# Kernel tuning notes

Measured on AMD Instinct MI355X. Metric: run time of the kernel, lower is better.

## Reference

```python
import jax, jax.numpy as jnp
import numpy as np

U = 100000          # unique pillars
N = 2 * U           # voxels (2 per pillar -> unq_cnt==2, mask all True)
NUM_BINS = 32       # z bins
C_IN = 5
C_HID = 32          # out_channels // 2 in conv1d MLP
C_OUT = 64
R = 4               # channel-attention reduction
K = 7               # bin-attention conv kernel


def setup_inputs() -> dict:
    key = jax.random.key(0)
    ks = jax.random.split(key, 12)
    voxel_features = jax.random.normal(ks[0], (N, C_IN), jnp.float32)
    # each pillar p owns voxels 2p, 2p+1 placed in two distinct bins -> no scatter collision
    bins = (jnp.arange(N, dtype=jnp.int32) % NUM_BINS)
    voxel_coords = jnp.zeros((N, 4), jnp.int32).at[:, 1].set(bins)
    unq_coords = jnp.arange(U, dtype=jnp.int32)
    unq_inv = jnp.arange(N, dtype=jnp.int32) // 2
    unq_cnt = jnp.full((U,), 2, jnp.int32)
    s = 0.3
    return {
        'voxel_features': voxel_features,
        'voxel_coords': voxel_coords,
        'unq_coords': unq_coords,
        'unq_inv': unq_inv,
        'unq_cnt': unq_cnt,
        # up_dimension MLP (Linear(5,32) -> relu -> Linear(32,64))
        'W1': jax.random.normal(ks[1], (C_IN, C_HID), jnp.float32) * s,
        'b1': jnp.zeros((C_HID,), jnp.float32),
        'W2': jax.random.normal(ks[2], (C_HID, C_OUT), jnp.float32) * s,
        'b2': jnp.zeros((C_OUT,), jnp.float32),
        # ZBAM channel-attention shared MLP
        'Wc1': jax.random.normal(ks[3], (C_OUT, C_OUT // R), jnp.float32) * s,
        'bc1': jnp.zeros((C_OUT // R,), jnp.float32),
        'Wc2': jax.random.normal(ks[4], (C_OUT // R, C_OUT), jnp.float32) * s,
        'bc2': jnp.zeros((C_OUT,), jnp.float32),
        # ZBAM bin (spatial) attention: conv1d over bins, 2->1 channels, kernel 7
        'Wsp': jax.random.normal(ks[5], (1, 2, K), jnp.float32) * s,
        'bsp': jnp.zeros((1,), jnp.float32),
    }


def _cbam_forward(voxel_features, W1, b1, W2, b2, Wc1, bc1, Wc2, bc2, Wsp, bsp,
                  voxel_coords, unq_coords, unq_inv, unq_cnt):
    n_pillars = unq_coords.shape[0]
    # --- binning: scatter voxels into (pillar, z-bin) slots ---
    src = jnp.zeros((n_pillars, NUM_BINS, voxel_features.shape[1]), voxel_features.dtype)
    src = src.at[unq_inv, voxel_coords[:, 1]].set(voxel_features)
    occupied_mask = unq_cnt >= 2  # all True by construction -> src[mask] == src
    # --- up_dimension MLP: (U, bins, 5) -> (U, bins, 64) ---
    x = jax.nn.relu(src @ W1 + b1) @ W2 + b2
    x = jnp.transpose(x, (0, 2, 1))  # (U, C, bins)
    # --- ZBAM channel attention ---
    avg_p = x.mean(axis=2)
    max_p = x.max(axis=2)
    mlp = lambda v: jax.nn.relu(v @ Wc1 + bc1) @ Wc2 + bc2
    att_c = jax.nn.sigmoid(mlp(avg_p) + mlp(max_p))  # (U, C)
    x = x * att_c[:, :, None]
    # --- ZBAM bin attention (conv over z-bins) ---
    s = jnp.stack([x.mean(axis=1), x.max(axis=1)], axis=1)  # (U, 2, bins)
    att_s = jax.lax.conv_general_dilated(
        s, Wsp, window_strides=(1,), padding=[(K // 2, K // 2)],
        dimension_numbers=('NCH', 'OIH', 'NCH')) + bsp  # (U, 1, bins)
    x = x * jax.nn.sigmoid(att_s)
    # --- max-pool over bins ---
    return x.max(axis=2), occupied_mask


def reference(voxel_features, voxel_coords, unq_coords, unq_inv, unq_cnt,
              W1, b1, W2, b2, Wc1, bc1, Wc2, bc2, Wsp, bsp):
    return _cbam_forward(voxel_features, W1, b1, W2, b2, Wc1, bc1, Wc2, bc2,
                         Wsp, bsp, voxel_coords, unq_coords, unq_inv, unq_cnt)
```

## Files before the change

kernel.cpp:

```cpp
#include <hip/hip_runtime.h>
#include <math.h>


#define CO 64

__device__ __forceinline__ float sgm(float x) {
  return 1.0f / (1.0f + __expf(-x));
}
template <int PAT>
__device__ __forceinline__ float qadd(float s) {
  int t = __builtin_amdgcn_update_dpp(0, __builtin_bit_cast(int, s),
                                      PAT, 0xf, 0xf, true);
  return s + __builtin_bit_cast(float, t);
}
template <int PAT>
__device__ __forceinline__ float qmaxd(float m) {
  int t = __builtin_amdgcn_update_dpp(__builtin_bit_cast(int, m),
                                      __builtin_bit_cast(int, m),
                                      PAT, 0xf, 0xf, false);
  return fmaxf(m, __builtin_bit_cast(float, t));
}
template <int PAT>
__device__ __forceinline__ float qmind(float m) {
  int t = __builtin_amdgcn_update_dpp(__builtin_bit_cast(int, m),
                                      __builtin_bit_cast(int, m),
                                      PAT, 0xf, 0xf, false);
  return fminf(m, __builtin_bit_cast(float, t));
}
__device__ __forceinline__ float qsum4(float s) { return qadd<0x4E>(qadd<0xB1>(s)); }
__device__ __forceinline__ float qmax4(float m) { return qmaxd<0x4E>(qmaxd<0xB1>(m)); }
__device__ __forceinline__ float qmin4(float m) { return qmind<0x4E>(qmind<0xB1>(m)); }
__device__ __forceinline__ void drain_lds() {
  __builtin_amdgcn_wave_barrier();
  __builtin_amdgcn_s_waitcnt(0xC07F);
  __builtin_amdgcn_wave_barrier();
}

__global__ __launch_bounds__(256) void pack_kernel(
    const float* __restrict__ vf, const int* __restrict__ vcoord,
    const int* __restrict__ unq_inv, float* __restrict__ pvox, int n) {
  int i = blockIdx.x * blockDim.x + threadIdx.x;
  if (i >= n) return;
  int p = unq_inv[i];
  int slot = (i > 0 && unq_inv[i - 1] == p) ? 1 : 0;
  float* dst = pvox + 8 * (size_t)(2 * p + slot);
#pragma unroll
  for (int k = 0; k < 5; ++k) dst[k] = vf[5 * i + k];
  ((int*)dst)[5] = vcoord[4 * i + 1];
}

__global__ __launch_bounds__(256) void cbam_kernel(
    const float* __restrict__ pvox, const int* __restrict__ unq_cnt,
    const float* __restrict__ W1, const float* __restrict__ b1,
    const float* __restrict__ W2, const float* __restrict__ b2,
    const float* __restrict__ Wc1, const float* __restrict__ bc1,
    const float* __restrict__ Wc2, const float* __restrict__ bc2,
    const float* __restrict__ Wsp, const float* __restrict__ bsp,
    float* __restrict__ out, int U) {
  __shared__ __align__(16) float w2b[2176];
  __shared__ __align__(16) float wc1b[1024];
  __shared__ __align__(16) float wc2b[1024];
  __shared__ __align__(16) float c0b[64], b2b[64], bc2b[64], bc1b[16];
  __shared__ __align__(16) float wsmx[64];
  __shared__ __align__(16) float wtab[16];
  __shared__ __align__(16) float hbuf[4][1152];

  const int tid = threadIdx.x;

  for (int i = tid; i < 2048; i += 256) w2b[(i >> 6) * 68 + (i & 63)] = W2[i];
  for (int i = tid; i < 1024; i += 256) wc1b[i] = Wc1[i];
  for (int i = tid; i < 1024; i += 256) wc2b[i] = Wc2[(i & 15) * 64 + (i >> 4)];
  if (tid < 64) { b2b[tid] = b2[tid]; bc2b[tid] = bc2[tid]; }
  if (tid < 16) bc1b[tid] = bc1[tid];
  if (tid < 32) {
    float sm = 0.0f, sx = 0.0f;
    for (int k = 0; k < 7; ++k)
      if ((unsigned)(tid + k - 3) < 32u) { sm += Wsp[k]; sx += Wsp[7 + k]; }
    wsmx[2 * tid] = sm; wsmx[2 * tid + 1] = sx;
  }
  if (tid < 8) {
    float a = 0.0f, b = 0.0f;
    if (tid < 7) { a = Wsp[tid]; b = Wsp[7 + tid]; }
    wtab[2 * tid] = a; wtab[2 * tid + 1] = b;
  }
  __syncthreads();
  if (tid < 64) {
    float c = b2b[tid];
    for (int j = 0; j < 32; ++j) c += fmaxf(b1[j], 0.0f) * w2b[j * 68 + tid];
    c0b[tid] = c;
  }
  __syncthreads();

  const int wv = tid >> 6, lane = tid & 63;
  const int P0 = (blockIdx.x * 4 + wv) * 16;
  if (P0 >= U) return;
  float* const hb = hbuf[wv];

  {
    const int j32 = lane & 31, vh = lane >> 5;
    float w1r[5];
#pragma unroll
    for (int i = 0; i < 5; ++i) w1r[i] = W1[i * 32 + j32];
    const float b1r = b1[j32];
    const float4* pv4 = (const float4*)pvox;
    const int vmax = 2 * U - 1;
#pragma unroll
    for (int v = 0; v < 16; ++v) {
      int vg = 2 * P0 + 16 * vh + v;
      vg = vg < vmax ? vg : vmax;
      float4 g1 = pv4[2 * vg];
      float4 g2 = pv4[2 * vg + 1];
      float h = b1r + g1.x * w1r[0] + g1.y * w1r[1] + g1.z * w1r[2] +
                g1.w * w1r[3] + g2.x * w1r[4];
      hb[(16 * vh + v) * 36 + j32] = fmaxf(h, 0.0f);
    }
  }
  drain_lds();

  const int q = lane & 3, pp = lane >> 2;
  const int pg = P0 + pp;
  const int pc = pg < U ? pg : (U - 1);
  const int cnt = unq_cnt[pc];
  const bool has2 = (cnt >= 2);
  const int* pvi = (const int*)pvox;
  const int b0 = pvi[(size_t)(2 * pc) * 8 + 5] & 31;
  const int b1raw = pvi[(size_t)(2 * pc + 1) * 8 + 5];
  const int b1e = has2 ? (b1raw & 31) : 64;

  float y0[16], y1[16];
  const float4* b2b4 = (const float4*)b2b;
#pragma unroll
  for (int kb = 0; kb < 4; ++kb) {
    float4 w = b2b4[q * 4 + kb];
    y0[4 * kb] = w.x; y0[4 * kb + 1] = w.y; y0[4 * kb + 2] = w.z; y0[4 * kb + 3] = w.w;
    y1[4 * kb] = w.x; y1[4 * kb + 1] = w.y; y1[4 * kb + 2] = w.z; y1[4 * kb + 3] = w.w;
  }
  const float4* hb4 = (const float4*)hb;
  const float4* w2b4 = (const float4*)w2b;
#pragma unroll
  for (int jb = 0; jb < 8; ++jb) {
    float4 h0 = hb4[(2 * pp) * 9 + jb];
    float4 h1 = hb4[(2 * pp + 1) * 9 + jb];
    float h0a[4] = {h0.x, h0.y, h0.z, h0.w};
    float h1a[4] = {h1.x, h1.y, h1.z, h1.w};
#pragma unroll
    for (int jj = 0; jj < 4; ++jj) {
      const int j = 4 * jb + jj;
#pragma unroll
      for (int kb = 0; kb < 4; ++kb) {
        float4 w = w2b4[17 * j + 4 * q + kb];
        y0[4 * kb]     += h0a[jj] * w.x; y0[4 * kb + 1] += h0a[jj] * w.y;
        y0[4 * kb + 2] += h0a[jj] * w.z; y0[4 * kb + 3] += h0a[jj] * w.w;
        y1[4 * kb]     += h1a[jj] * w.x; y1[4 * kb + 1] += h1a[jj] * w.y;
        y1[4 * kb + 2] += h1a[jj] * w.z; y1[4 * kb + 3] += h1a[jj] * w.w;
      }
    }
  }
#pragma unroll
  for (int k = 0; k < 16; ++k) y1[k] = has2 ? y1[k] : y0[k];

  float ha[16] = {0}, hm[16] = {0};
  const float kf = has2 ? 30.0f : 31.0f;
  const float inv32 = 1.0f / 32.0f;
  const float4* c04 = (const float4*)c0b;
  const float4* wc14 = (const float4*)wc1b;
#pragma unroll
  for (int kb = 0; kb < 4; ++kb) {
    float4 cq = c04[q * 4 + kb];
    float c0a[4] = {cq.x, cq.y, cq.z, cq.w};
#pragma unroll
    for (int i = 0; i < 4; ++i) {
      const int k = 4 * kb + i;
      const float c0v = c0a[i];
      const float sumy = y0[k] + (has2 ? y1[k] : 0.0f);
      const float avg = fmaf(c0v, kf, sumy) * inv32;
      const float mxv = fmaxf(fmaxf(y0[k], y1[k]), c0v);
#pragma unroll
      for (int jb = 0; jb < 4; ++jb) {
        float4 w = wc14[(16 * q + k) * 4 + jb];
        ha[4 * jb]     += avg * w.x; ha[4 * jb + 1] += avg * w.y;
        ha[4 * jb + 2] += avg * w.z; ha[4 * jb + 3] += avg * w.w;
        hm[4 * jb]     += mxv * w.x; hm[4 * jb + 1] += mxv * w.y;
        hm[4 * jb + 2] += mxv * w.z; hm[4 * jb + 3] += mxv * w.w;
      }
    }
  }
  float g[16];
  const float4* bc14 = (const float4*)bc1b;
#pragma unroll
  for (int jb = 0; jb < 4; ++jb) {
    float4 bb = bc14[jb];
    float bba[4] = {bb.x, bb.y, bb.z, bb.w};
#pragma unroll
    for (int i = 0; i < 4; ++i) {
      const int j = 4 * jb + i;
      const float sa = qsum4(ha[j]) + bba[i];
      const float sm = qsum4(hm[j]) + bba[i];
      g[j] = fmaxf(sa, 0.0f) + fmaxf(sm, 0.0f);
    }
  }

  float attc[16];
  float sc = 0.0f, mc = -3.0e38f;
  float sy0 = 0.0f, my0 = -3.0e38f, sy1 = 0.0f, my1 = -3.0e38f;
  const float4* wc24 = (const float4*)wc2b;
  const float4* bc24 = (const float4*)bc2b;
#pragma unroll
  for (int kb = 0; kb < 4; ++kb) {
    float4 cq = c04[q * 4 + kb];
    float4 bq = bc24[q * 4 + kb];
    float c0a[4] = {cq.x, cq.y, cq.z, cq.w};
    float b2a[4] = {bq.x, bq.y, bq.z, bq.w};
#pragma unroll
    for (int i = 0; i < 4; ++i) {
      const int k = 4 * kb + i;
      float pre = 2.0f * b2a[i];
#pragma unroll
      for (int jb = 0; jb < 4; ++jb) {
        float4 w = wc24[(16 * q + k) * 4 + jb];
        pre += g[4 * jb] * w.x + g[4 * jb + 1] * w.y +
               g[4 * jb + 2] * w.z + g[4 * jb + 3] * w.w;
      }
      const float a = sgm(pre);
      attc[k] = a;
      const float pc0 = a * c0a[i], py0 = a * y0[k], py1 = a * y1[k];
      sc += pc0;  mc = fmaxf(mc, pc0);
      sy0 += py0; my0 = fmaxf(my0, py0);
      sy1 += py1; my1 = fmaxf(my1, py1);
    }
  }
  sc = qsum4(sc);   mc = qmax4(mc);
  sy0 = qsum4(sy0); my0 = qmax4(my0);
  sy1 = qsum4(sy1); my1 = qmax4(my1);

  const float inv64 = 1.0f / 64.0f;
  const float Mn = sc * inv64, Mx = mc;
  const float dm0 = (sy0 - sc) * inv64, dx0 = my0 - mc;
  const float dm1 = (sy1 - sc) * inv64, dx1 = my1 - mc;
  const float bspr = bsp[0];
  const float2* ws2 = (const float2*)wsmx;
  const float2* wt2 = (const float2*)wtab;
  float maxE = -3.0e38f, minE = 3.0e38f, sv0 = -3.0e38f, sv1 = -3.0e38f;
#pragma unroll
  for (int k = 0; k < 8; ++k) {
    const int b = 8 * q + k;
    float2 ws = ws2[b];
    float acc = bspr + Mn * ws.x + Mx * ws.y;
    int k0 = b0 - b + 3;  k0 = ((unsigned)k0 <= 6u) ? k0 : 7;
    int k1 = b1e - b + 3; k1 = ((unsigned)k1 <= 6u) ? k1 : 7;
    float2 w0 = wt2[k0];
    float2 w1v = wt2[k1];
    acc += dm0 * w0.x + dx0 * w0.y + dm1 * w1v.x + dx1 * w1v.y;
    const bool o0 = (b == b0), o1 = (b == b1e);
    const bool oc = o0 || o1;
    maxE = fmaxf(maxE, oc ? -3.0e38f : acc);
    minE = fminf(minE, oc ?  3.0e38f : acc);
    sv0 = o0 ? acc : sv0;
    sv1 = o1 ? acc : sv1;
  }
  maxE = qmax4(maxE); minE = qmin4(minE);
  sv0 = qmax4(sv0);   sv1 = qmax4(sv1);
  const float sig0 = sgm(sv0);
  const float sig1 = has2 ? sgm(sv1) : sig0;
  const float sE = sgm(maxE), sI = sgm(minE);

  if (pg < U) {
    float4* ov = (float4*)(out + (size_t)pg * CO + 16 * q);
#pragma unroll
    for (int kb = 0; kb < 4; ++kb) {
      float4 cq = c04[q * 4 + kb];
      float c0a[4] = {cq.x, cq.y, cq.z, cq.w};
      float rr[4];
#pragma unroll
      for (int i = 0; i < 4; ++i) {
        const int k = 4 * kb + i;
        const float c0v = c0a[i];
        const float sel = (c0v >= 0.0f) ? sE : sI;
        const float m = fmaxf(fmaxf(y0[k] * sig0, y1[k] * sig1), c0v * sel);
        rr[i] = attc[k] * m;
      }
      float4 r; r.x = rr[0]; r.y = rr[1]; r.z = rr[2]; r.w = rr[3];
      ov[kb] = r;
    }
    if (q == 0) out[(size_t)U * CO + pg] = has2 ? 1.0f : 0.0f;
  }
}

extern "C" void kernel_launch(void* const* d_in, const int* in_sizes, int n_in,
                              void* d_out, int out_size, void* d_ws, size_t ws_size,
                              hipStream_t stream) {
  const float* vf      = (const float*)d_in[0];
  const int*   vcoord  = (const int*)d_in[1];
  const int*   unq_inv = (const int*)d_in[3];
  const int*   unq_cnt = (const int*)d_in[4];
  const float* W1  = (const float*)d_in[5];
  const float* b1  = (const float*)d_in[6];
  const float* W2  = (const float*)d_in[7];
  const float* b2  = (const float*)d_in[8];
  const float* Wc1 = (const float*)d_in[9];
  const float* bc1 = (const float*)d_in[10];
  const float* Wc2 = (const float*)d_in[11];
  const float* bc2 = (const float*)d_in[12];
  const float* Wsp = (const float*)d_in[13];
  const float* bsp = (const float*)d_in[14];

  const int N = in_sizes[3];
  const int U = in_sizes[4];

  float* pvox = (float*)d_ws;

  pack_kernel<<<(N + 255) / 256, 256, 0, stream>>>(vf, vcoord, unq_inv, pvox, N);

  const int waves = (U + 15) / 16;
  const int blocks = (waves + 3) / 4;
  cbam_kernel<<<blocks, 256, 0, stream>>>(
      pvox, unq_cnt, W1, b1, W2, b2, Wc1, bc1, Wc2, bc2, Wsp, bsp,
      (float*)d_out, U);
}
```

Before: 155.5 us.

## Make CBAM kernel persistent with grid-stride waves and reorder LDS layouts

The main kernel now launches a capped grid of 1024 blocks, and each wave loops over 16-pillar groups in grid-stride fashion. The per-block weight staging into shared memory and the W1 register loads now happen once per wave rather than once per group. The hidden-activation rows and the Wc1/Wc2 shared-memory layouts are permuted, intended to reduce LDS bank conflicts, and the hidden-row reads are software-prefetched one step ahead. The cost is fewer resident blocks, which may reduce latency hiding, plus an extra LDS drain per loop iteration.

After: 147.6 us. 5.1% less time.

```diff
diff --git a/kernel.cpp b/kernel.cpp
--- a/kernel.cpp
+++ b/kernel.cpp
@@ -56,7 +56,7 @@
     const float* __restrict__ Wc1, const float* __restrict__ bc1,
     const float* __restrict__ Wc2, const float* __restrict__ bc2,
     const float* __restrict__ Wsp, const float* __restrict__ bsp,
-    float* __restrict__ out, int U) {
+    float* __restrict__ out, int U, int ngroups, int totalWaves) {
   __shared__ __align__(16) float w2b[2176];
   __shared__ __align__(16) float wc1b[1024];
   __shared__ __align__(16) float wc2b[1024];
@@ -68,8 +68,11 @@
   const int tid = threadIdx.x;
 
   for (int i = tid; i < 2048; i += 256) w2b[(i >> 6) * 68 + (i & 63)] = W2[i];
-  for (int i = tid; i < 1024; i += 256) wc1b[i] = Wc1[i];
-  for (int i = tid; i < 1024; i += 256) wc2b[i] = Wc2[(i & 15) * 64 + (i >> 4)];
+  for (int i = tid; i < 1024; i += 256) {
+    int ch = i >> 4, j = i & 15, qq = ch >> 4, k = ch & 15;
+    wc1b[(4 * k + qq) * 16 + j] = Wc1[i];
+    wc2b[(4 * k + qq) * 16 + j] = Wc2[j * 64 + ch];
+  }
   if (tid < 64) { b2b[tid] = b2[tid]; bc2b[tid] = bc2[tid]; }
   if (tid < 16) bc1b[tid] = bc1[tid];
   if (tid < 32) {
@@ -92,197 +95,210 @@
   __syncthreads();
 
   const int wv = tid >> 6, lane = tid & 63;
-  const int P0 = (blockIdx.x * 4 + wv) * 16;
-  if (P0 >= U) return;
+  const int wave0 = blockIdx.x * 4 + wv;
   float* const hb = hbuf[wv];
 
-  {
-    const int j32 = lane & 31, vh = lane >> 5;
-    float w1r[5];
-#pragma unroll
-    for (int i = 0; i < 5; ++i) w1r[i] = W1[i * 32 + j32];
-    const float b1r = b1[j32];
-    const float4* pv4 = (const float4*)pvox;
-    const int vmax = 2 * U - 1;
-#pragma unroll
-    for (int v = 0; v < 16; ++v) {
-      int vg = 2 * P0 + 16 * vh + v;
-      vg = vg < vmax ? vg : vmax;
-      float4 g1 = pv4[2 * vg];
-      float4 g2 = pv4[2 * vg + 1];
-      float h = b1r + g1.x * w1r[0] + g1.y * w1r[1] + g1.z * w1r[2] +
-                g1.w * w1r[3] + g2.x * w1r[4];
-      hb[(16 * vh + v) * 36 + j32] = fmaxf(h, 0.0f);
-    }
-  }
-  drain_lds();
+  const int j32 = lane & 31, vh = lane >> 5;
+  float w1r[5];
+#pragma unroll
+  for (int i = 0; i < 5; ++i) w1r[i] = W1[i * 32 + j32];
+  const float b1r = b1[j32];
 
   const int q = lane & 3, pp = lane >> 2;
-  const int pg = P0 + pp;
-  const int pc = pg < U ? pg : (U - 1);
-  const int cnt = unq_cnt[pc];
-  const bool has2 = (cnt >= 2);
-  const int* pvi = (const int*)pvox;
-  const int b0 = pvi[(size_t)(2 * pc) * 8 + 5] & 31;
-  const int b1raw = pvi[(size_t)(2 * pc + 1) * 8 + 5];
-  const int b1e = has2 ? (b1raw & 31) : 64;
-
-  float y0[16], y1[16];
-  const float4* b2b4 = (const float4*)b2b;
-#pragma unroll
-  for (int kb = 0; kb < 4; ++kb) {
-    float4 w = b2b4[q * 4 + kb];
-    y0[4 * kb] = w.x; y0[4 * kb + 1] = w.y; y0[4 * kb + 2] = w.z; y0[4 * kb + 3] = w.w;
-    y1[4 * kb] = w.x; y1[4 * kb + 1] = w.y; y1[4 * kb + 2] = w.z; y1[4 * kb + 3] = w.w;
-  }
-  const float4* hb4 = (const float4*)hb;
-  const float4* w2b4 = (const float4*)w2b;
-#pragma unroll
-  for (int jb = 0; jb < 8; ++jb) {
-    float4 h0 = hb4[(2 * pp) * 9 + jb];
-    float4 h1 = hb4[(2 * pp + 1) * 9 + jb];
-    float h0a[4] = {h0.x, h0.y, h0.z, h0.w};
-    float h1a[4] = {h1.x, h1.y, h1.z, h1.w};
-#pragma unroll
-    for (int jj = 0; jj < 4; ++jj) {
-      const int j = 4 * jb + jj;
-#pragma unroll
-      for (int kb = 0; kb < 4; ++kb) {
-        float4 w = w2b4[17 * j + 4 * q + kb];
-        y0[4 * kb]     += h0a[jj] * w.x; y0[4 * kb + 1] += h0a[jj] * w.y;
-        y0[4 * kb + 2] += h0a[jj] * w.z; y0[4 * kb + 3] += h0a[jj] * w.w;
-        y1[4 * kb]     += h1a[jj] * w.x; y1[4 * kb + 1] += h1a[jj] * w.y;
-        y1[4 * kb + 2] += h1a[jj] * w.z; y1[4 * kb + 3] += h1a[jj] * w.w;
-      }
-    }
-  }
-#pragma unroll
-  for (int k = 0; k < 16; ++k) y1[k] = has2 ? y1[k] : y0[k];
-
-  float ha[16] = {0}, hm[16] = {0};
-  const float kf = has2 ? 30.0f : 31.0f;
-  const float inv32 = 1.0f / 32.0f;
-  const float4* c04 = (const float4*)c0b;
-  const float4* wc14 = (const float4*)wc1b;
-#pragma unroll
-  for (int kb = 0; kb < 4; ++kb) {
-    float4 cq = c04[q * 4 + kb];
-    float c0a[4] = {cq.x, cq.y, cq.z, cq.w};
-#pragma unroll
-    for (int i = 0; i < 4; ++i) {
-      const int k = 4 * kb + i;
-      const float c0v = c0a[i];
-      const float sumy = y0[k] + (has2 ? y1[k] : 0.0f);
-      const float avg = fmaf(c0v, kf, sumy) * inv32;
-      const float mxv = fmaxf(fmaxf(y0[k], y1[k]), c0v);
-#pragma unroll
-      for (int jb = 0; jb < 4; ++jb) {
-        float4 w = wc14[(16 * q + k) * 4 + jb];
-        ha[4 * jb]     += avg * w.x; ha[4 * jb + 1] += avg * w.y;
-        ha[4 * jb + 2] += avg * w.z; ha[4 * jb + 3] += avg * w.w;
-        hm[4 * jb]     += mxv * w.x; hm[4 * jb + 1] += mxv * w.y;
-        hm[4 * jb + 2] += mxv * w.z; hm[4 * jb + 3] += mxv * w.w;
-      }
-    }
-  }
-  float g[16];
-  const float4* bc14 = (const float4*)bc1b;
-#pragma unroll
-  for (int jb = 0; jb < 4; ++jb) {
-    float4 bb = bc14[jb];
-    float bba[4] = {bb.x, bb.y, bb.z, bb.w};
-#pragma unroll
-    for (int i = 0; i < 4; ++i) {
-      const int j = 4 * jb + i;
-      const float sa = qsum4(ha[j]) + bba[i];
-      const float sm = qsum4(hm[j]) + bba[i];
-      g[j] = fmaxf(sa, 0.0f) + fmaxf(sm, 0.0f);
-    }
-  }
-
-  float attc[16];
-  float sc = 0.0f, mc = -3.0e38f;
-  float sy0 = 0.0f, my0 = -3.0e38f, sy1 = 0.0f, my1 = -3.0e38f;
-  const float4* wc24 = (const float4*)wc2b;
-  const float4* bc24 = (const float4*)bc2b;
-#pragma unroll
-  for (int kb = 0; kb < 4; ++kb) {
-    float4 cq = c04[q * 4 + kb];
-    float4 bq = bc24[q * 4 + kb];
-    float c0a[4] = {cq.x, cq.y, cq.z, cq.w};
-    float b2a[4] = {bq.x, bq.y, bq.z, bq.w};
-#pragma unroll
-    for (int i = 0; i < 4; ++i) {
-      const int k = 4 * kb + i;
-      float pre = 2.0f * b2a[i];
-#pragma unroll
-      for (int jb = 0; jb < 4; ++jb) {
-        float4 w = wc24[(16 * q + k) * 4 + jb];
-        pre += g[4 * jb] * w.x + g[4 * jb + 1] * w.y +
-               g[4 * jb + 2] * w.z + g[4 * jb + 3] * w.w;
-      }
-      const float a = sgm(pre);
-      attc[k] = a;
-      const float pc0 = a * c0a[i], py0 = a * y0[k], py1 = a * y1[k];
-      sc += pc0;  mc = fmaxf(mc, pc0);
-      sy0 += py0; my0 = fmaxf(my0, py0);
-      sy1 += py1; my1 = fmaxf(my1, py1);
-    }
-  }
-  sc = qsum4(sc);   mc = qmax4(mc);
-  sy0 = qsum4(sy0); my0 = qmax4(my0);
-  sy1 = qsum4(sy1); my1 = qmax4(my1);
-
-  const float inv64 = 1.0f / 64.0f;
-  const float Mn = sc * inv64, Mx = mc;
-  const float dm0 = (sy0 - sc) * inv64, dx0 = my0 - mc;
-  const float dm1 = (sy1 - sc) * inv64, dx1 = my1 - mc;
-  const float bspr = bsp[0];
-  const float2* ws2 = (const float2*)wsmx;
-  const float2* wt2 = (const float2*)wtab;
-  float maxE = -3.0e38f, minE = 3.0e38f, sv0 = -3.0e38f, sv1 = -3.0e38f;
-#pragma unroll
-  for (int k = 0; k < 8; ++k) {
-    const int b = 8 * q + k;
-    float2 ws = ws2[b];
-    float acc = bspr + Mn * ws.x + Mx * ws.y;
-    int k0 = b0 - b + 3;  k0 = ((unsigned)k0 <= 6u) ? k0 : 7;
-    int k1 = b1e - b + 3; k1 = ((unsigned)k1 <= 6u) ? k1 : 7;
-    float2 w0 = wt2[k0];
-    float2 w1v = wt2[k1];
-    acc += dm0 * w0.x + dx0 * w0.y + dm1 * w1v.x + dx1 * w1v.y;
-    const bool o0 = (b == b0), o1 = (b == b1e);
-    const bool oc = o0 || o1;
-    maxE = fmaxf(maxE, oc ? -3.0e38f : acc);
-    minE = fminf(minE, oc ?  3.0e38f : acc);
-    sv0 = o0 ? acc : sv0;
-    sv1 = o1 ? acc : sv1;
-  }
-  maxE = qmax4(maxE); minE = qmin4(minE);
-  sv0 = qmax4(sv0);   sv1 = qmax4(sv1);
-  const float sig0 = sgm(sv0);
-  const float sig1 = has2 ? sgm(sv1) : sig0;
-  const float sE = sgm(maxE), sI = sgm(minE);
-
-  if (pg < U) {
-    float4* ov = (float4*)(out + (size_t)pg * CO + 16 * q);
+
+  for (int grp = wave0; grp < ngroups; grp += totalWaves) {
+    const int P0 = grp * 16;
+
+    {
+      const float4* pv4 = (const float4*)pvox;
+      const int vmax = 2 * U - 1;
+#pragma unroll
+      for (int v = 0; v < 16; ++v) {
+        int vg = 2 * P0 + 16 * vh + v;
+        vg = vg < vmax ? vg : vmax;
+        float4 g1 = pv4[2 * vg];
+        float4 g2 = pv4[2 * vg + 1];
+        float h = b1r + g1.x * w1r[0] + g1.y * w1r[1] + g1.z * w1r[2] +
+                  g1.w * w1r[3] + g2.x * w1r[4];
+        const int row = (v & 1) * 16 + 8 * vh + (v >> 1);
+        hb[row * 36 + j32] = fmaxf(h, 0.0f);
+      }
+    }
+    drain_lds();
+
+    const int pg = P0 + pp;
+    const int pc = pg < U ? pg : (U - 1);
+    const int cnt = unq_cnt[pc];
+    const bool has2 = (cnt >= 2);
+    const int* pvi = (const int*)pvox;
+    const int b0 = pvi[(size_t)(2 * pc) * 8 + 5] & 31;
+    const int b1raw = pvi[(size_t)(2 * pc + 1) * 8 + 5];
+    const int b1e = has2 ? (b1raw & 31) : 64;
+
+    float y0[16], y1[16];
+    const float4* b2b4 = (const float4*)b2b;
+#pragma unroll
+    for (int kb = 0; kb < 4; ++kb) {
+      float4 w = b2b4[q * 4 + kb];
+      y0[4 * kb] = w.x; y0[4 * kb + 1] = w.y; y0[4 * kb + 2] = w.z; y0[4 * kb + 3] = w.w;
+      y1[4 * kb] = w.x; y1[4 * kb + 1] = w.y; y1[4 * kb + 2] = w.z; y1[4 * kb + 3] = w.w;
+    }
+    const float4* hb4 = (const float4*)hb;
+    const float4* w2b4 = (const float4*)w2b;
+    float4 h0c = hb4[pp * 9];
+    float4 h1c = hb4[(16 + pp) * 9];
+#pragma unroll
+    for (int jb = 0; jb < 8; ++jb) {
+      float4 h0n, h1n;
+      if (jb < 7) {
+        h0n = hb4[pp * 9 + jb + 1];
+        h1n = hb4[(16 + pp) * 9 + jb + 1];
+      }
+      float h0a[4] = {h0c.x, h0c.y, h0c.z, h0c.w};
+      float h1a[4] = {h1c.x, h1c.y, h1c.z, h1c.w};
+#pragma unroll
+      for (int jj = 0; jj < 4; ++jj) {
+        const int j = 4 * jb + jj;
+#pragma unroll
+        for (int kb = 0; kb < 4; ++kb) {
+          float4 w = w2b4[17 * j + 4 * q + kb];
+          y0[4 * kb]     += h0a[jj] * w.x; y0[4 * kb + 1] += h0a[jj] * w.y;
+          y0[4 * kb + 2] += h0a[jj] * w.z; y0[4 * kb + 3] += h0a[jj] * w.w;
+          y1[4 * kb]     += h1a[jj] * w.x; y1[4 * kb + 1] += h1a[jj] * w.y;
+          y1[4 * kb + 2] += h1a[jj] * w.z; y1[4 * kb + 3] += h1a[jj] * w.w;
+        }
+      }
+      h0c = h0n; h1c = h1n;
+    }
+#pragma unroll
+    for (int k = 0; k < 16; ++k) y1[k] = has2 ? y1[k] : y0[k];
+
+    float ha[16] = {0}, hm[16] = {0};
+    const float kf = has2 ? 30.0f : 31.0f;
+    const float inv32 = 1.0f / 32.0f;
+    const float4* c04 = (const float4*)c0b;
+    const float4* wc14 = (const float4*)wc1b;
 #pragma unroll
     for (int kb = 0; kb < 4; ++kb) {
       float4 cq = c04[q * 4 + kb];
       float c0a[4] = {cq.x, cq.y, cq.z, cq.w};
-      float rr[4];
 #pragma unroll
       for (int i = 0; i < 4; ++i) {
         const int k = 4 * kb + i;
         const float c0v = c0a[i];
-        const float sel = (c0v >= 0.0f) ? sE : sI;
-        const float m = fmaxf(fmaxf(y0[k] * sig0, y1[k] * sig1), c0v * sel);
-        rr[i] = attc[k] * m;
-      }
-      float4 r; r.x = rr[0]; r.y = rr[1]; r.z = rr[2]; r.w = rr[3];
-      ov[kb] = r;
-    }
-    if (q == 0) out[(size_t)U * CO + pg] = has2 ? 1.0f : 0.0f;
+        const float sumy = y0[k] + (has2 ? y1[k] : 0.0f);
+        const float avg = fmaf(c0v, kf, sumy) * inv32;
+        const float mxv = fmaxf(fmaxf(y0[k], y1[k]), c0v);
+#pragma unroll
+        for (int jb = 0; jb < 4; ++jb) {
+          float4 w = wc14[(4 * k + q) * 4 + jb];
+          ha[4 * jb]     += avg * w.x; ha[4 * jb + 1] += avg * w.y;
+          ha[4 * jb + 2] += avg * w.z; ha[4 * jb + 3] += avg * w.w;
+          hm[4 * jb]     += mxv * w.x; hm[4 * jb + 1] += mxv * w.y;
+          hm[4 * jb + 2] += mxv * w.z; hm[4 * jb + 3] += mxv * w.w;
+        }
+      }
+    }
+    float g[16];
+    const float4* bc14 = (const float4*)bc1b;
+#pragma unroll
+    for (int jb = 0; jb < 4; ++jb) {
+      float4 bb = bc14[jb];
+      float bba[4] = {bb.x, bb.y, bb.z, bb.w};
+#pragma unroll
+      for (int i = 0; i < 4; ++i) {
+        const int j = 4 * jb + i;
+        const float sa = qsum4(ha[j]) + bba[i];
+        const float sm = qsum4(hm[j]) + bba[i];
+        g[j] = fmaxf(sa, 0.0f) + fmaxf(sm, 0.0f);
+      }
+    }
+
+    float attc[16];
+    float sc = 0.0f, mc = -3.0e38f;
+    float sy0 = 0.0f, my0 = -3.0e38f, sy1 = 0.0f, my1 = -3.0e38f;
+    const float4* wc24 = (const float4*)wc2b;
+    const float4* bc24 = (const float4*)bc2b;
+#pragma unroll
+    for (int kb = 0; kb < 4; ++kb) {
+      float4 cq = c04[q * 4 + kb];
+      float4 bq = bc24[q * 4 + kb];
+      float c0a[4] = {cq.x, cq.y, cq.z, cq.w};
+      float b2a[4] = {bq.x, bq.y, bq.z, bq.w};
+#pragma unroll
+      for (int i = 0; i < 4; ++i) {
+        const int k = 4 * kb + i;
+        float pre = 2.0f * b2a[i];
+#pragma unroll
+        for (int jb = 0; jb < 4; ++jb) {
+          float4 w = wc24[(4 * k + q) * 4 + jb];
+          pre += g[4 * jb] * w.x + g[4 * jb + 1] * w.y +
+                 g[4 * jb + 2] * w.z + g[4 * jb + 3] * w.w;
+        }
+        const float a = sgm(pre);
+        attc[k] = a;
+        const float pc0 = a * c0a[i], py0 = a * y0[k], py1 = a * y1[k];
+        sc += pc0;  mc = fmaxf(mc, pc0);
+        sy0 += py0; my0 = fmaxf(my0, py0);
+        sy1 += py1; my1 = fmaxf(my1, py1);
+      }
+    }
+    sc = qsum4(sc);   mc = qmax4(mc);
+    sy0 = qsum4(sy0); my0 = qmax4(my0);
+    sy1 = qsum4(sy1); my1 = qmax4(my1);
+
+    const float inv64 = 1.0f / 64.0f;
+    const float Mn = sc * inv64, Mx = mc;
+    const float dm0 = (sy0 - sc) * inv64, dx0 = my0 - mc;
+    const float dm1 = (sy1 - sc) * inv64, dx1 = my1 - mc;
+    const float bspr = bsp[0];
+    const float2* ws2 = (const float2*)wsmx;
+    const float2* wt2 = (const float2*)wtab;
+    float maxE = -3.0e38f, minE = 3.0e38f, sv0 = -3.0e38f, sv1 = -3.0e38f;
+#pragma unroll
+    for (int k = 0; k < 8; ++k) {
+      const int b = 8 * q + k;
+      float2 ws = ws2[b];
+      float acc = bspr + Mn * ws.x + Mx * ws.y;
+      int k0 = b0 - b + 3;  k0 = ((unsigned)k0 <= 6u) ? k0 : 7;
+      int k1 = b1e - b + 3; k1 = ((unsigned)k1 <= 6u) ? k1 : 7;
+      float2 w0 = wt2[k0];
+      float2 w1v = wt2[k1];
+      acc += dm0 * w0.x + dx0 * w0.y + dm1 * w1v.x + dx1 * w1v.y;
+      const bool o0 = (b == b0), o1 = (b == b1e);
+      const bool oc = o0 || o1;
+      maxE = fmaxf(maxE, oc ? -3.0e38f : acc);
+      minE = fminf(minE, oc ?  3.0e38f : acc);
+      sv0 = o0 ? acc : sv0;
+      sv1 = o1 ? acc : sv1;
+    }
+    maxE = qmax4(maxE); minE = qmin4(minE);
+    sv0 = qmax4(sv0);   sv1 = qmax4(sv1);
+    const float sig0 = sgm(sv0);
+    const float sig1 = has2 ? sgm(sv1) : sig0;
+    const float sE = sgm(maxE), sI = sgm(minE);
+
+    if (pg < U) {
+      float4* ov = (float4*)(out + (size_t)pg * CO + 16 * q);
+#pragma unroll
+      for (int kb = 0; kb < 4; ++kb) {
+        float4 cq = c04[q * 4 + kb];
+        float c0a[4] = {cq.x, cq.y, cq.z, cq.w};
+        float rr[4];
+#pragma unroll
+        for (int i = 0; i < 4; ++i) {
+          const int k = 4 * kb + i;
+          const float c0v = c0a[i];
+          const float sel = (c0v >= 0.0f) ? sE : sI;
+          const float m = fmaxf(fmaxf(y0[k] * sig0, y1[k] * sig1), c0v * sel);
+          rr[i] = attc[k] * m;
+        }
+        float4 r; r.x = rr[0]; r.y = rr[1]; r.z = rr[2]; r.w = rr[3];
+        ov[kb] = r;
+      }
+      if (q == 0) out[(size_t)U * CO + pg] = has2 ? 1.0f : 0.0f;
+    }
+    drain_lds();
   }
 }
 
@@ -311,9 +327,12 @@
 
   pack_kernel<<<(N + 255) / 256, 256, 0, stream>>>(vf, vcoord, unq_inv, pvox, N);
 
-  const int waves = (U + 15) / 16;
-  const int blocks = (waves + 3) / 4;
+  const int ngroups = (U + 15) / 16;
+  int blocks = 1024;
+  const int maxBlocks = (ngroups + 3) / 4;
+  if (blocks > maxBlocks) blocks = maxBlocks;
+  const int totalWaves = blocks * 4;
   cbam_kernel<<<blocks, 256, 0, stream>>>(
       pvox, unq_cnt, W1, b1, W2, b2, Wc1, bc1, Wc2, bc2, Wsp, bsp,
-      (float*)d_out, U);
-}
+      (float*)d_out, U, ngroups, totalWaves);
+}
```
